# Performance work log

Hardware: AMD Instinct MI355X
Metric: run time of the kernel (lower is better)

## Reference

```python
import jax, jax.numpy as jnp
import numpy as np

EMBED = 1024
DFF = 4096


def _layernorm(x, g, b, eps=1e-5):
    mu = jnp.mean(x, axis=-1, keepdims=True)
    var = jnp.var(x, axis=-1, keepdims=True)
    return (x - mu) * jax.lax.rsqrt(var + eps) * g + b


def setup_inputs() -> dict:
    key = jax.random.key(0)
    ks = jax.random.split(key, 14)
    s = 1.0 / np.sqrt(EMBED)
    sf = 1.0 / np.sqrt(DFF)
    d = {
        "src": jax.random.normal(ks[0], (4, 2048, EMBED), dtype=jnp.float32),
        "Wq": jax.random.uniform(ks[1], (EMBED, EMBED), jnp.float32, -s, s),
        "bq": jnp.zeros((EMBED,), jnp.float32),
        "Wk": jax.random.uniform(ks[2], (EMBED, EMBED), jnp.float32, -s, s),
        "bk": jnp.zeros((EMBED,), jnp.float32),
        "Wv": jax.random.uniform(ks[3], (EMBED, EMBED), jnp.float32, -s, s),
        "bv": jnp.zeros((EMBED,), jnp.float32),
        "Wo": jax.random.uniform(ks[4], (EMBED, EMBED), jnp.float32, -s, s),
        "bo": jnp.zeros((EMBED,), jnp.float32),
        "W1": jax.random.uniform(ks[5], (EMBED, DFF), jnp.float32, -s, s),
        "b1": jnp.zeros((DFF,), jnp.float32),
        "W2": jax.random.uniform(ks[6], (DFF, EMBED), jnp.float32, -sf, sf),
        "b2": jnp.zeros((EMBED,), jnp.float32),
        "g1": jnp.ones((EMBED,), jnp.float32),
        "be1": jnp.zeros((EMBED,), jnp.float32),
        "g2": jnp.ones((EMBED,), jnp.float32),
        "be2": jnp.zeros((EMBED,), jnp.float32),
    }
    return d


def reference(src, Wq, bq, Wk, bk, Wv, bv, Wo, bo, W1, b1, W2, b2, g1, be1, g2, be2):
    # Q/K/V projections: [b, s, d]
    Q = src @ Wq + bq
    K = src @ Wk + bk
    V = src @ Wv + bv
    # Single-head, UNSCALED attention (faithful to source: no 1/sqrt(d), num_heads unused)
    scores = jnp.einsum("bqd,bkd->bqk", Q, K)  # [b, s, s]
    weights = jax.nn.softmax(scores, axis=-1)
    attn = jnp.einsum("bqk,bkd->bqd", weights, V)
    attn = attn @ Wo + bo
    x = _layernorm(src + attn, g1, be1)
    ff = jax.nn.relu(x @ W1 + b1) @ W2 + b2
    return _layernorm(x + ff, g2, be2)
```

## Files before the change

### kernel.cpp

```cpp
#include <hip/hip_runtime.h>
#include <stdint.h>

typedef unsigned short u16;
typedef _Float16 v8h __attribute__((ext_vector_type(8)));
typedef float v4f __attribute__((ext_vector_type(4)));

static __device__ __forceinline__ float h2f(u16 u) {
    union { u16 s; _Float16 h; } v; v.s = u; return (float)v.h;
}
static __device__ __forceinline__ u16 f2h(float f) {
    union { u16 s; _Float16 h; } v; v.h = (_Float16)f; return v.s;
}

static __device__ __forceinline__ void gload_lds16(const u16* g, const u16* l) {
    __builtin_amdgcn_global_load_lds(
        (const __attribute__((address_space(1))) uint32_t*)(uintptr_t)g,
        (__attribute__((address_space(3))) uint32_t*)(uintptr_t)l,
        16, 0, 0);
}

__global__ __launch_bounds__(256) void cvt_f16(const float* __restrict__ in,
                                               u16* __restrict__ out, int n8) {
    const int i = blockIdx.x * 256 + threadIdx.x;
    if (i >= n8) return;
    const float4 a = ((const float4*)in)[2 * i];
    const float4 b = ((const float4*)in)[2 * i + 1];
    u16 o[8] = {f2h(a.x), f2h(a.y), f2h(a.z), f2h(a.w),
                f2h(b.x), f2h(b.y), f2h(b.z), f2h(b.w)};
    *(uint4*)(out + (size_t)i * 8) = *(const uint4*)o;
}

__global__ __launch_bounds__(256) void transpose_all(
    const float* __restrict__ Wq, const float* __restrict__ Wk,
    const float* __restrict__ Wv, const float* __restrict__ Wo,
    const float* __restrict__ W1, const float* __restrict__ W2,
    u16* __restrict__ WqkvT, u16* __restrict__ WoT,
    u16* __restrict__ W1T, u16* __restrict__ W2T)
{
    int t = blockIdx.x;
    const float* in; u16* out; long ldi, ldo; int xt;
    if (t < 1024)      {            in = Wq; out = WqkvT;               ldi = 1024; ldo = 1024; xt = 32; }
    else if (t < 2048) { t -= 1024; in = Wk; out = WqkvT + 1024*1024;   ldi = 1024; ldo = 1024; xt = 32; }
    else if (t < 3072) { t -= 2048; in = Wv; out = WqkvT + 2*1024*1024; ldi = 1024; ldo = 1024; xt = 32; }
    else if (t < 4096) { t -= 3072; in = Wo; out = WoT;                 ldi = 1024; ldo = 1024; xt = 32; }
    else if (t < 8192) { t -= 4096; in = W1; out = W1T;                 ldi = 4096; ldo = 1024; xt = 128; }
    else               { t -= 8192; in = W2; out = W2T;                 ldi = 1024; ldo = 4096; xt = 32; }
    const int c0 = (t % xt) * 32, r0 = (t / xt) * 32;
    __shared__ float tile[32][33];
    for (int i = threadIdx.y; i < 32; i += 8)
        tile[i][threadIdx.x] = in[(long)(r0 + i) * ldi + c0 + threadIdx.x];
    __syncthreads();
    for (int i = threadIdx.y; i < 32; i += 8)
        out[(long)(c0 + i) * ldo + r0 + threadIdx.x] = f2h(tile[threadIdx.x][i]);
}

template<int OMODE, int BIAS, bool RELU, int NX, int NY, int NZ>
__global__ __launch_bounds__(512, 4) void gemm256n(
    const u16* __restrict__ A, long lda, long Asb,
    const u16* __restrict__ B, long ldb, long Bsb,
    void* __restrict__ Cv, long ldc, long Csb, u16* __restrict__ C1,
    const float* __restrict__ bias, const float* __restrict__ bias2,
    const float* __restrict__ bias3, int K)
{
    constexpr int NWG = NX * NY * NZ;
    static_assert(NWG % 8 == 0, "XCD swizzle needs nwg % 8 == 0");
    alignas(16) __shared__ u16 As[4 * 8192];
    alignas(16) __shared__ u16 Bs[2 * 4096];

    const int tid = threadIdx.x;
    const int lane = tid & 63, wave = tid >> 6;
    const int l16 = lane & 15, quad = lane >> 4;
    const int wm = wave >> 1;
    const int wn = wave & 1;

    const int lin = blockIdx.x;
    const int tl = (lin & 7) * (NWG / 8) + (lin >> 3);
    const int xe = tl % NX;
    const int ye = (tl / NX) % NY;
    const int zb = tl / (NX * NY);
    const long m0 = (long)ye * 256;
    const long n0 = (long)xe * 128;

    const u16* Aop = A + (long)zb * Asb;
    const u16* Bop = B + (long)zb * Bsb;

    const int srow = tid >> 2;
    const int sq = (tid & 3) ^ ((tid >> 3) & 3);
    const long gaofs0 = (m0 + srow) * lda + sq * 8;
    const long gaofs1 = gaofs0 + 128 * lda;
    const long gbofs0 = (n0 + srow) * ldb + sq * 8;
    const int wv512n = wave * 512;

    const int swzE = (quad ^ ((l16 >> 1) & 3)) * 8;
    const int aRow = (wm * 64 + l16) * 32 + swzE;
    const int bRow = (wn * 64 + l16) * 32 + swzE;

    v4f acc[4][4];
#pragma unroll
    for (int i = 0; i < 4; ++i)
#pragma unroll
        for (int j = 0; j < 4; ++j)
            acc[i][j] = (v4f){0.f, 0.f, 0.f, 0.f};
    v8h bf[4];

#define STAGE_A(RIDX, KP) do { \
        u16* lb_ = As + (RIDX) * 8192 + wv512n; \
        gload_lds16(Aop + gaofs0 + (KP), lb_); \
        gload_lds16(Aop + gaofs1 + (KP), lb_ + 4096); } while (0)
#define STAGE_B(SLOT, KP) do { \
        gload_lds16(Bop + gbofs0 + (KP), Bs + (SLOT) * 4096 + wv512n); } while (0)

#define PHASE(BUF, KH, CH, EVENW, STG) { \
        if (EVENW) asm volatile("s_waitcnt vmcnt(2)" ::: "memory"); \
        const u16* Ar_ = As + ((BUF) * 2 + (KH)) * 8192 + aRow + (CH) * 1024; \
        v8h af0 = *(const v8h*)(Ar_); \
        v8h af1 = *(const v8h*)(Ar_ + 512); \
        if ((CH) == 0) { \
            const u16* Br_ = Bs + (KH) * 4096 + bRow; \
            bf[0] = *(const v8h*)(Br_); \
            bf[1] = *(const v8h*)(Br_ + 512); \
            bf[2] = *(const v8h*)(Br_ + 1024); \
            bf[3] = *(const v8h*)(Br_ + 1536); \
        } \
        STG; \
        __builtin_amdgcn_s_barrier(); \
        asm volatile("s_waitcnt lgkmcnt(0)" ::: "memory"); \
        __builtin_amdgcn_s_setprio(1); \
        acc[(CH)*2+0][0] = __builtin_amdgcn_mfma_f32_16x16x32_f16(af0, bf[0], acc[(CH)*2+0][0], 0, 0, 0); \
        acc[(CH)*2+0][1] = __builtin_amdgcn_mfma_f32_16x16x32_f16(af0, bf[1], acc[(CH)*2+0][1], 0, 0, 0); \
        acc[(CH)*2+0][2] = __builtin_amdgcn_mfma_f32_16x16x32_f16(af0, bf[2], acc[(CH)*2+0][2], 0, 0, 0); \
        acc[(CH)*2+0][3] = __builtin_amdgcn_mfma_f32_16x16x32_f16(af0, bf[3], acc[(CH)*2+0][3], 0, 0, 0); \
        acc[(CH)*2+1][0] = __builtin_amdgcn_mfma_f32_16x16x32_f16(af1, bf[0], acc[(CH)*2+1][0], 0, 0, 0); \
        acc[(CH)*2+1][1] = __builtin_amdgcn_mfma_f32_16x16x32_f16(af1, bf[1], acc[(CH)*2+1][1], 0, 0, 0); \
        acc[(CH)*2+1][2] = __builtin_amdgcn_mfma_f32_16x16x32_f16(af1, bf[2], acc[(CH)*2+1][2], 0, 0, 0); \
        acc[(CH)*2+1][3] = __builtin_amdgcn_mfma_f32_16x16x32_f16(af1, bf[3], acc[(CH)*2+1][3], 0, 0, 0); \
        __builtin_amdgcn_s_setprio(0); \
        __builtin_amdgcn_s_barrier(); \
    }

    STAGE_A(0, 0);  STAGE_B(0, 0);
    STAGE_A(1, 32); STAGE_B(1, 32);
    STAGE_A(2, 64);
    asm volatile("s_waitcnt vmcnt(5)" ::: "memory");
    __builtin_amdgcn_s_barrier();

    const int NT = K >> 7;
#pragma unroll 1
    for (int t = 0; t < NT; ++t) {
        const long kb = (long)t * 128;
        long kp2  = kb + 128; if (kp2  >= K) kp2  = 0;
        long kp2b = kb + 160; if (kp2b >= K) kp2b = 0;
        long kp3  = kb + 192; if (kp3  >= K) kp3  = 0;

        PHASE(0, 0, 0, false, STAGE_A(3, kb + 96))
        PHASE(0, 0, 1, true,  STAGE_B(0, kb + 64))
        PHASE(0, 1, 0, false, STAGE_A(0, kp2))
        PHASE(0, 1, 1, true,  STAGE_B(1, kb + 96))
        PHASE(1, 0, 0, false, STAGE_A(1, kp2b))
        PHASE(1, 0, 1, true,  STAGE_B(0, kp2))
        PHASE(1, 1, 0, false, STAGE_A(2, kp3))
        PHASE(1, 1, 1, true,  STAGE_B(1, kp2b))
    }

    asm volatile("s_waitcnt vmcnt(0) lgkmcnt(0)" ::: "memory");
    __builtin_amdgcn_s_barrier();

#undef PHASE
#undef STAGE_A
#undef STAGE_B

    float bv[4];
#pragma unroll
    for (int j = 0; j < 4; ++j) {
        const long col = n0 + wn * 64 + j * 16 + l16;
        if (BIAS == 0) bv[j] = 0.f;
        else if (BIAS == 1) bv[j] = bias[col];
        else {
            const int sel = (int)(col >> 10);
            const float* bp = sel == 0 ? bias : (sel == 1 ? bias2 : bias3);
            bv[j] = bp[col & 1023];
        }
    }

    if (OMODE == 3 && n0 >= 2048) {
        const long bb = m0 >> 11, mb = m0 & 2047;
        u16* C = C1 + bb * Csb;
#pragma unroll
        for (int j = 0; j < 4; ++j) {
            const long col = n0 - 2048 + wn * 64 + j * 16 + l16;
            u16* pc = C + col * 2048 + mb + wm * 64 + quad * 4;
#pragma unroll
            for (int i = 0; i < 4; ++i) {
                u16 o[4];
#pragma unroll
                for (int r = 0; r < 4; ++r) {
                    float val = acc[i][j][r] + bv[j];
                    if (RELU) val = fmaxf(val, 0.f);
                    o[r] = f2h(val);
                }
                *(uint2*)(pc + i * 16) = *(const uint2*)o;
            }
        }
    } else {
        const long cb = (OMODE == 3 ? 0 : (long)zb * Csb)
                      + (m0 + wm * 64 + quad * 4) * ldc + (n0 + wn * 64 + l16);
        u16* p0 = (u16*)Cv + cb;
#pragma unroll
        for (int i = 0; i < 4; ++i)
#pragma unroll
            for (int r = 0; r < 4; ++r) {
                u16* prow = p0 + (long)(i * 16 + r) * ldc;
#pragma unroll
                for (int j = 0; j < 4; ++j) {
                    float val = acc[i][j][r] + bv[j];
                    if (RELU) val = fmaxf(val, 0.f);
                    prow[j * 16] = f2h(val);
                }
            }
    }
}

__global__ __launch_bounds__(256) void softmax_rows(u16* __restrict__ S) {
    const long row = blockIdx.x;
    u16* p = S + row * 2048;
    const int t = threadIdx.x;
    const int lane = t & 63, wv = t >> 6;

    union { uint4 u; u16 h[8]; } ld;
    ld.u = *(const uint4*)(p + t * 8);
    float v[8];
    float mx = -1e30f;
#pragma unroll
    for (int i = 0; i < 8; ++i) { v[i] = h2f(ld.h[i]); mx = fmaxf(mx, v[i]); }
#pragma unroll
    for (int o = 1; o < 64; o <<= 1) mx = fmaxf(mx, __shfl_xor(mx, o, 64));
    __shared__ float cw[4], cs[4];
    if (lane == 0) cw[wv] = mx;
    __syncthreads();
    mx = fmaxf(fmaxf(cw[0], cw[1]), fmaxf(cw[2], cw[3]));

    float sum = 0.f;
#pragma unroll
    for (int i = 0; i < 8; ++i) { v[i] = __expf(v[i] - mx); sum += v[i]; }
#pragma unroll
    for (int o = 1; o < 64; o <<= 1) sum += __shfl_xor(sum, o, 64);
    if (lane == 0) cs[wv] = sum;
    __syncthreads();
    sum = (cs[0] + cs[1]) + (cs[2] + cs[3]);

    const float inv = 1.f / sum;
#pragma unroll
    for (int i = 0; i < 8; ++i) ld.h[i] = f2h(v[i] * inv);
    *(uint4*)(p + t * 8) = ld.u;
}

__global__ __launch_bounds__(256) void ln_one(
    const float* __restrict__ a, const u16* __restrict__ bb,
    const float* __restrict__ g, const float* __restrict__ be,
    u16* __restrict__ out16)
{
    const long base = (long)blockIdx.x * 1024;
    const int t = threadIdx.x;
    const int lane = t & 63, wv = t >> 6;
    const int c0 = t * 4;

    const float4 av = *(const float4*)(a + base + c0);
    union { uint2 u; u16 h[4]; } bv;
    bv.u = *(const uint2*)(bb + base + c0);
    float v[4] = {av.x + h2f(bv.h[0]), av.y + h2f(bv.h[1]),
                  av.z + h2f(bv.h[2]), av.w + h2f(bv.h[3])};
    float s = 0.f, ss = 0.f;
#pragma unroll
    for (int i = 0; i < 4; ++i) { s += v[i]; ss += v[i] * v[i]; }
#pragma unroll
    for (int o = 1; o < 64; o <<= 1) { s += __shfl_xor(s, o, 64); ss += __shfl_xor(ss, o, 64); }
    __shared__ float cs[4], css[4];
    if (lane == 0) { cs[wv] = s; css[wv] = ss; }
    __syncthreads();
    s  = (cs[0] + cs[1]) + (cs[2] + cs[3]);
    ss = (css[0] + css[1]) + (css[2] + css[3]);

    const float mean = s * (1.f / 1024.f);
    const float var = ss * (1.f / 1024.f) - mean * mean;
    const float rstd = rsqrtf(var + 1e-5f);
    const float4 gv = *(const float4*)(g + c0);
    const float4 bev = *(const float4*)(be + c0);
    u16 o[4] = {f2h((v[0] - mean) * rstd * gv.x + bev.x),
                f2h((v[1] - mean) * rstd * gv.y + bev.y),
                f2h((v[2] - mean) * rstd * gv.z + bev.z),
                f2h((v[3] - mean) * rstd * gv.w + bev.w)};
    *(uint2*)(out16 + base + c0) = *(const uint2*)o;
}

__global__ __launch_bounds__(256) void ln_two(
    const u16* __restrict__ a, const u16* __restrict__ bb,
    const float* __restrict__ g, const float* __restrict__ be,
    float* __restrict__ out)
{
    const long base = (long)blockIdx.x * 1024;
    const int t = threadIdx.x;
    const int lane = t & 63, wv = t >> 6;
    const int c0 = t * 4;

    union { uint2 u; u16 h[4]; } avu, bvu;
    avu.u = *(const uint2*)(a + base + c0);
    bvu.u = *(const uint2*)(bb + base + c0);
    float v[4];
    float s = 0.f, ss = 0.f;
#pragma unroll
    for (int i = 0; i < 4; ++i) {
        v[i] = h2f(avu.h[i]) + h2f(bvu.h[i]);
        s += v[i]; ss += v[i] * v[i];
    }
#pragma unroll
    for (int o = 1; o < 64; o <<= 1) { s += __shfl_xor(s, o, 64); ss += __shfl_xor(ss, o, 64); }
    __shared__ float cs[4], css[4];
    if (lane == 0) { cs[wv] = s; css[wv] = ss; }
    __syncthreads();
    s  = (cs[0] + cs[1]) + (cs[2] + cs[3]);
    ss = (css[0] + css[1]) + (css[2] + css[3]);

    const float mean = s * (1.f / 1024.f);
    const float var = ss * (1.f / 1024.f) - mean * mean;
    const float rstd = rsqrtf(var + 1e-5f);
    const float4 gv = *(const float4*)(g + c0);
    const float4 bev = *(const float4*)(be + c0);
    float4 o;
    o.x = (v[0] - mean) * rstd * gv.x + bev.x;
    o.y = (v[1] - mean) * rstd * gv.y + bev.y;
    o.z = (v[2] - mean) * rstd * gv.z + bev.z;
    o.w = (v[3] - mean) * rstd * gv.w + bev.w;
    *(float4*)(out + base + c0) = o;
}

extern "C" void kernel_launch(void* const* d_in, const int* in_sizes, int n_in,
                              void* d_out, int out_size, void* d_ws, size_t ws_size,
                              hipStream_t stream) {
    (void)in_sizes; (void)n_in; (void)out_size; (void)ws_size;
    constexpr long S = 2048, E = 1024, F = 4096, M = 8192;

    const float* src = (const float*)d_in[0];
    const float* Wq  = (const float*)d_in[1];
    const float* bq  = (const float*)d_in[2];
    const float* Wk  = (const float*)d_in[3];
    const float* bk  = (const float*)d_in[4];
    const float* Wv  = (const float*)d_in[5];
    const float* bv  = (const float*)d_in[6];
    const float* Wo  = (const float*)d_in[7];
    const float* bo  = (const float*)d_in[8];
    const float* W1  = (const float*)d_in[9];
    const float* b1  = (const float*)d_in[10];
    const float* W2  = (const float*)d_in[11];
    const float* b2  = (const float*)d_in[12];
    const float* g1  = (const float*)d_in[13];
    const float* be1 = (const float*)d_in[14];
    const float* g2  = (const float*)d_in[15];
    const float* be2 = (const float*)d_in[16];

    char* ws = (char*)d_ws;
    size_t off = 0;
    auto take = [&](size_t bytes) {
        char* p = ws + off;
        off += (bytes + 255) & ~(size_t)255;
        return p;
    };
    const size_t MB16 = 16777216;
    u16*   srcH  = (u16*)take(MB16);
    u16*   WqkvT = (u16*)take(3 * E * E * 2);
    u16*   WoT   = (u16*)take(E * E * 2);
    u16*   W1T   = (u16*)take(F * E * 2);
    u16*   W2T   = (u16*)take(E * F * 2);
    char*  B0    = take(2 * MB16);
    char*  B1    = take(MB16);
    char*  B2    = take(4ull * S * S * 4);
    char*  B3    = take(MB16);
    char*  B4    = take(MB16);

    u16*   QK    = (u16*)B0;
    u16*   VT    = (u16*)B1;
    u16*   Sh    = (u16*)B2;
    u16*   hf    = (u16*)B2;
    u16*   attn  = (u16*)B3;
    u16*   xh    = (u16*)B3;
    u16*   attnO = (u16*)B4;
    u16*   ffO   = (u16*)B4;

    dim3 blk(256), blk5(512), tb(32, 8);

    cvt_f16<<<dim3(M * E / 8 / 256), blk, 0, stream>>>(src, srcH, M * E / 8);

    transpose_all<<<dim3(12288), tb, 0, stream>>>(Wq, Wk, Wv, Wo, W1, W2,
                                                  WqkvT, WoT, W1T, W2T);

    gemm256n<3, 3, false, 24, 32, 1><<<dim3(24 * 32), blk5, 0, stream>>>(
        srcH, E, 0, WqkvT, E, 0, QK, 2 * E, E * S, VT, bq, bk, bv, E);

    gemm256n<0, 0, false, 16, 8, 4><<<dim3(16 * 8 * 4), blk5, 0, stream>>>(
        QK, 2 * E, S * 2 * E, QK + E, 2 * E, S * 2 * E,
        Sh, S, S * S, nullptr, nullptr, nullptr, nullptr, E);

    softmax_rows<<<dim3(M), blk, 0, stream>>>(Sh);

    gemm256n<0, 0, false, 8, 8, 4><<<dim3(8 * 8 * 4), blk5, 0, stream>>>(
        Sh, S, S * S, VT, S, E * S,
        attn, E, S * E, nullptr, nullptr, nullptr, nullptr, S);

    gemm256n<0, 1, false, 8, 32, 1><<<dim3(8 * 32), blk5, 0, stream>>>(
        attn, E, 0, WoT, E, 0, attnO, E, 0, nullptr, bo, nullptr, nullptr, E);

    ln_one<<<dim3(M), blk, 0, stream>>>(src, attnO, g1, be1, xh);

    gemm256n<0, 1, true, 32, 32, 1><<<dim3(32 * 32), blk5, 0, stream>>>(
        xh, E, 0, W1T, E, 0, hf, F, 0, nullptr, b1, nullptr, nullptr, E);

    gemm256n<0, 1, false, 8, 32, 1><<<dim3(8 * 32), blk5, 0, stream>>>(
        hf, F, 0, W2T, F, 0, ffO, E, 0, nullptr, b2, nullptr, nullptr, F);

    ln_two<<<dim3(M), blk, 0, stream>>>(xh, ffO, g2, be2, (float*)d_out);
}
```

Before: 481.5 us.

## Use 4 waves per GEMM block with 128x64 per-wave tiles

Halves the GEMM workgroup from 512 to 256 threads (4 waves), so each wave now computes a 128x64 output subtile with 32 accumulators instead of 16. Each thread issues twice as many global-to-LDS loads per stage, and the vmcnt waits are adjusted to match. The aim is more MFMA work per LDS fragment load and fewer waves to barrier-synchronise. The cost is higher register pressure (128 accumulator VGPRs) and launch bounds of (256,2), which may lower occupancy and latency hiding.

```diff
diff --git a/kernel.cpp b/kernel.cpp
--- a/kernel.cpp
+++ b/kernel.cpp
@@ -55,7 +55,7 @@
 }
 
 template<int OMODE, int BIAS, bool RELU, int NX, int NY, int NZ>
-__global__ __launch_bounds__(512, 4) void gemm256n(
+__global__ __launch_bounds__(256, 2) void gemm256n(
     const u16* __restrict__ A, long lda, long Asb,
     const u16* __restrict__ B, long ldb, long Bsb,
     void* __restrict__ Cv, long ldc, long Csb, u16* __restrict__ C1,
@@ -87,17 +87,16 @@
     const int srow = tid >> 2;
     const int sq = (tid & 3) ^ ((tid >> 3) & 3);
     const long gaofs0 = (m0 + srow) * lda + sq * 8;
-    const long gaofs1 = gaofs0 + 128 * lda;
     const long gbofs0 = (n0 + srow) * ldb + sq * 8;
     const int wv512n = wave * 512;
 
     const int swzE = (quad ^ ((l16 >> 1) & 3)) * 8;
-    const int aRow = (wm * 64 + l16) * 32 + swzE;
+    const int aRow = (wm * 128 + l16) * 32 + swzE;
     const int bRow = (wn * 64 + l16) * 32 + swzE;
 
-    v4f acc[4][4];
-#pragma unroll
-    for (int i = 0; i < 4; ++i)
+    v4f acc[8][4];
+#pragma unroll
+    for (int i = 0; i < 8; ++i)
 #pragma unroll
         for (int j = 0; j < 4; ++j)
             acc[i][j] = (v4f){0.f, 0.f, 0.f, 0.f};
@@ -106,15 +105,21 @@
 #define STAGE_A(RIDX, KP) do { \
         u16* lb_ = As + (RIDX) * 8192 + wv512n; \
         gload_lds16(Aop + gaofs0 + (KP), lb_); \
-        gload_lds16(Aop + gaofs1 + (KP), lb_ + 4096); } while (0)
+        gload_lds16(Aop + gaofs0 + 64 * lda + (KP), lb_ + 2048); \
+        gload_lds16(Aop + gaofs0 + 128 * lda + (KP), lb_ + 4096); \
+        gload_lds16(Aop + gaofs0 + 192 * lda + (KP), lb_ + 6144); } while (0)
 #define STAGE_B(SLOT, KP) do { \
-        gload_lds16(Bop + gbofs0 + (KP), Bs + (SLOT) * 4096 + wv512n); } while (0)
+        u16* lb_ = Bs + (SLOT) * 4096 + wv512n; \
+        gload_lds16(Bop + gbofs0 + (KP), lb_); \
+        gload_lds16(Bop + gbofs0 + 64 * ldb + (KP), lb_ + 2048); } while (0)
 
 #define PHASE(BUF, KH, CH, EVENW, STG) { \
-        if (EVENW) asm volatile("s_waitcnt vmcnt(2)" ::: "memory"); \
-        const u16* Ar_ = As + ((BUF) * 2 + (KH)) * 8192 + aRow + (CH) * 1024; \
+        if (EVENW) asm volatile("s_waitcnt vmcnt(4)" ::: "memory"); \
+        const u16* Ar_ = As + ((BUF) * 2 + (KH)) * 8192 + aRow + (CH) * 2048; \
         v8h af0 = *(const v8h*)(Ar_); \
         v8h af1 = *(const v8h*)(Ar_ + 512); \
+        v8h af2 = *(const v8h*)(Ar_ + 1024); \
+        v8h af3 = *(const v8h*)(Ar_ + 1536); \
         if ((CH) == 0) { \
             const u16* Br_ = Bs + (KH) * 4096 + bRow; \
             bf[0] = *(const v8h*)(Br_); \
@@ -126,14 +131,22 @@
         __builtin_amdgcn_s_barrier(); \
         asm volatile("s_waitcnt lgkmcnt(0)" ::: "memory"); \
         __builtin_amdgcn_s_setprio(1); \
-        acc[(CH)*2+0][0] = __builtin_amdgcn_mfma_f32_16x16x32_f16(af0, bf[0], acc[(CH)*2+0][0], 0, 0, 0); \
-        acc[(CH)*2+0][1] = __builtin_amdgcn_mfma_f32_16x16x32_f16(af0, bf[1], acc[(CH)*2+0][1], 0, 0, 0); \
-        acc[(CH)*2+0][2] = __builtin_amdgcn_mfma_f32_16x16x32_f16(af0, bf[2], acc[(CH)*2+0][2], 0, 0, 0); \
-        acc[(CH)*2+0][3] = __builtin_amdgcn_mfma_f32_16x16x32_f16(af0, bf[3], acc[(CH)*2+0][3], 0, 0, 0); \
-        acc[(CH)*2+1][0] = __builtin_amdgcn_mfma_f32_16x16x32_f16(af1, bf[0], acc[(CH)*2+1][0], 0, 0, 0); \
-        acc[(CH)*2+1][1] = __builtin_amdgcn_mfma_f32_16x16x32_f16(af1, bf[1], acc[(CH)*2+1][1], 0, 0, 0); \
-        acc[(CH)*2+1][2] = __builtin_amdgcn_mfma_f32_16x16x32_f16(af1, bf[2], acc[(CH)*2+1][2], 0, 0, 0); \
-        acc[(CH)*2+1][3] = __builtin_amdgcn_mfma_f32_16x16x32_f16(af1, bf[3], acc[(CH)*2+1][3], 0, 0, 0); \
+        acc[(CH)*4+0][0] = __builtin_amdgcn_mfma_f32_16x16x32_f16(af0, bf[0], acc[(CH)*4+0][0], 0, 0, 0); \
+        acc[(CH)*4+0][1] = __builtin_amdgcn_mfma_f32_16x16x32_f16(af0, bf[1], acc[(CH)*4+0][1], 0, 0, 0); \
+        acc[(CH)*4+0][2] = __builtin_amdgcn_mfma_f32_16x16x32_f16(af0, bf[2], acc[(CH)*4+0][2], 0, 0, 0); \
+        acc[(CH)*4+0][3] = __builtin_amdgcn_mfma_f32_16x16x32_f16(af0, bf[3], acc[(CH)*4+0][3], 0, 0, 0); \
+        acc[(CH)*4+1][0] = __builtin_amdgcn_mfma_f32_16x16x32_f16(af1, bf[0], acc[(CH)*4+1][0], 0, 0, 0); \
+        acc[(CH)*4+1][1] = __builtin_amdgcn_mfma_f32_16x16x32_f16(af1, bf[1], acc[(CH)*4+1][1], 0, 0, 0); \
+        acc[(CH)*4+1][2] = __builtin_amdgcn_mfma_f32_16x16x32_f16(af1, bf[2], acc[(CH)*4+1][2], 0, 0, 0); \
+        acc[(CH)*4+1][3] = __builtin_amdgcn_mfma_f32_16x16x32_f16(af1, bf[3], acc[(CH)*4+1][3], 0, 0, 0); \
+        acc[(CH)*4+2][0] = __builtin_amdgcn_mfma_f32_16x16x32_f16(af2, bf[0], acc[(CH)*4+2][0], 0, 0, 0); \
+        acc[(CH)*4+2][1] = __builtin_amdgcn_mfma_f32_16x16x32_f16(af2, bf[1], acc[(CH)*4+2][1], 0, 0, 0); \
+        acc[(CH)*4+2][2] = __builtin_amdgcn_mfma_f32_16x16x32_f16(af2, bf[2], acc[(CH)*4+2][2], 0, 0, 0); \
+        acc[(CH)*4+2][3] = __builtin_amdgcn_mfma_f32_16x16x32_f16(af2, bf[3], acc[(CH)*4+2][3], 0, 0, 0); \
+        acc[(CH)*4+3][0] = __builtin_amdgcn_mfma_f32_16x16x32_f16(af3, bf[0], acc[(CH)*4+3][0], 0, 0, 0); \
+        acc[(CH)*4+3][1] = __builtin_amdgcn_mfma_f32_16x16x32_f16(af3, bf[1], acc[(CH)*4+3][1], 0, 0, 0); \
+        acc[(CH)*4+3][2] = __builtin_amdgcn_mfma_f32_16x16x32_f16(af3, bf[2], acc[(CH)*4+3][2], 0, 0, 0); \
+        acc[(CH)*4+3][3] = __builtin_amdgcn_mfma_f32_16x16x32_f16(af3, bf[3], acc[(CH)*4+3][3], 0, 0, 0); \
         __builtin_amdgcn_s_setprio(0); \
         __builtin_amdgcn_s_barrier(); \
     }
@@ -141,7 +154,7 @@
     STAGE_A(0, 0);  STAGE_B(0, 0);
     STAGE_A(1, 32); STAGE_B(1, 32);
     STAGE_A(2, 64);
-    asm volatile("s_waitcnt vmcnt(5)" ::: "memory");
+    asm volatile("s_waitcnt vmcnt(10)" ::: "memory");
     __builtin_amdgcn_s_barrier();
 
     const int NT = K >> 7;
@@ -188,9 +201,9 @@
 #pragma unroll
         for (int j = 0; j < 4; ++j) {
             const long col = n0 - 2048 + wn * 64 + j * 16 + l16;
-            u16* pc = C + col * 2048 + mb + wm * 64 + quad * 4;
-#pragma unroll
-            for (int i = 0; i < 4; ++i) {
+            u16* pc = C + col * 2048 + mb + wm * 128 + quad * 4;
+#pragma unroll
+            for (int i = 0; i < 8; ++i) {
                 u16 o[4];
 #pragma unroll
                 for (int r = 0; r < 4; ++r) {
@@ -203,10 +216,10 @@
         }
     } else {
         const long cb = (OMODE == 3 ? 0 : (long)zb * Csb)
-                      + (m0 + wm * 64 + quad * 4) * ldc + (n0 + wn * 64 + l16);
+                      + (m0 + wm * 128 + quad * 4) * ldc + (n0 + wn * 64 + l16);
         u16* p0 = (u16*)Cv + cb;
 #pragma unroll
-        for (int i = 0; i < 4; ++i)
+        for (int i = 0; i < 8; ++i)
 #pragma unroll
             for (int r = 0; r < 4; ++r) {
                 u16* prow = p0 + (long)(i * 16 + r) * ldc;
@@ -385,35 +398,35 @@
     u16*   attnO = (u16*)B4;
     u16*   ffO   = (u16*)B4;
 
-    dim3 blk(256), blk5(512), tb(32, 8);
+    dim3 blk(256), tb(32, 8);
 
     cvt_f16<<<dim3(M * E / 8 / 256), blk, 0, stream>>>(src, srcH, M * E / 8);
 
     transpose_all<<<dim3(12288), tb, 0, stream>>>(Wq, Wk, Wv, Wo, W1, W2,
                                                   WqkvT, WoT, W1T, W2T);
 
-    gemm256n<3, 3, false, 24, 32, 1><<<dim3(24 * 32), blk5, 0, stream>>>(
+    gemm256n<3, 3, false, 24, 32, 1><<<dim3(24 * 32), blk, 0, stream>>>(
         srcH, E, 0, WqkvT, E, 0, QK, 2 * E, E * S, VT, bq, bk, bv, E);
 
-    gemm256n<0, 0, false, 16, 8, 4><<<dim3(16 * 8 * 4), blk5, 0, stream>>>(
+    gemm256n<0, 0, false, 16, 8, 4><<<dim3(16 * 8 * 4), blk, 0, stream>>>(
         QK, 2 * E, S * 2 * E, QK + E, 2 * E, S * 2 * E,
         Sh, S, S * S, nullptr, nullptr, nullptr, nullptr, E);
 
     softmax_rows<<<dim3(M), blk, 0, stream>>>(Sh);
 
-    gemm256n<0, 0, false, 8, 8, 4><<<dim3(8 * 8 * 4), blk5, 0, stream>>>(
+    gemm256n<0, 0, false, 8, 8, 4><<<dim3(8 * 8 * 4), blk, 0, stream>>>(
         Sh, S, S * S, VT, S, E * S,
         attn, E, S * E, nullptr, nullptr, nullptr, nullptr, S);
 
-    gemm256n<0, 1, false, 8, 32, 1><<<dim3(8 * 32), blk5, 0, stream>>>(
+    gemm256n<0, 1, false, 8, 32, 1><<<dim3(8 * 32), blk, 0, stream>>>(
         attn, E, 0, WoT, E, 0, attnO, E, 0, nullptr, bo, nullptr, nullptr, E);
 
     ln_one<<<dim3(M), blk, 0, stream>>>(src, attnO, g1, be1, xh);
 
-    gemm256n<0, 1, true, 32, 32, 1><<<dim3(32 * 32), blk5, 0, stream>>>(
+    gemm256n<0, 1, true, 32, 32, 1><<<dim3(32 * 32), blk, 0, stream>>>(
         xh, E, 0, W1T, E, 0, hf, F, 0, nullptr, b1, nullptr, nullptr, E);
 
-    gemm256n<0, 1, false, 8, 32, 1><<<dim3(8 * 32), blk5, 0, stream>>>(
+    gemm256n<0, 1, false, 8, 32, 1><<<dim3(8 * 32), blk, 0, stream>>>(
         hf, F, 0, W2T, F, 0, ffO, E, 0, nullptr, b2, nullptr, nullptr, F);
 
     ln_two<<<dim3(M), blk, 0, stream>>>(xh, ffO, g2, be2, (float*)d_out);
```

New measurement: 478.5 us. About the same (-0.6%).
